# Kernel optimization log

Hardware: AMD Instinct MI355X
Metric: run time of the kernel (lower is better)

The kernel has to match this reference:

```python
import jax, jax.numpy as jnp
import numpy as np
import math

B, S, U, H = 2, 2048, 1024, 16
DK = U // H  # 64


def setup_inputs() -> dict:
    key = jax.random.key(0)
    ks = jax.random.split(key, 12)
    scale = 1.0 / math.sqrt(U)
    inp = {
        "query": jax.random.normal(ks[0], (B, S, U), dtype=jnp.float32),
        "key": jax.random.normal(ks[1], (B, S, U), dtype=jnp.float32),
        "value": jax.random.normal(ks[2], (B, S, U), dtype=jnp.float32),
        # causal mask, broadcast over batch: 1 = attend, 0 = masked
        "mask": jnp.broadcast_to(jnp.tril(jnp.ones((S, S), dtype=bool)), (B, S, S)),
        # nn.Linear params (torch convention: y = x @ W.T + b)
        "Wq": jax.random.uniform(ks[3], (U, U), jnp.float32, -scale, scale),
        "bq": jax.random.uniform(ks[4], (U,), jnp.float32, -scale, scale),
        "Wk": jax.random.uniform(ks[5], (U, U), jnp.float32, -scale, scale),
        "bk": jax.random.uniform(ks[6], (U,), jnp.float32, -scale, scale),
        "Wv": jax.random.uniform(ks[7], (U, U), jnp.float32, -scale, scale),
        "bv": jax.random.uniform(ks[8], (U,), jnp.float32, -scale, scale),
        "Wo": jax.random.uniform(ks[9], (U, U), jnp.float32, -scale, scale),
        "bo": jax.random.uniform(ks[10], (U,), jnp.float32, -scale, scale),
    }
    return inp


def reference(query, key, value, mask, Wq, bq, Wk, bk, Wv, bv, Wo, bo):
    b = query.shape[0]
    # QKV projections -> [b, H, S, DK]
    q = (query @ Wq.T + bq).reshape(b, -1, H, DK).transpose(0, 2, 1, 3)
    k = (key @ Wk.T + bk).reshape(b, -1, H, DK).transpose(0, 2, 1, 3)
    v = (value @ Wv.T + bv).reshape(b, -1, H, DK).transpose(0, 2, 1, 3)
    # scaled dot-product scores [b, H, Sq, Sk]
    scores = jnp.einsum("bhqd,bhkd->bhqk", q, k) / math.sqrt(DK)
    scores = jnp.where(mask[:, None, :, :], scores, jnp.float32(-1e9))
    A = jax.nn.softmax(scores, axis=-1)
    # dropout is eval/identity (p effectively inactive in reference)
    Hout = jnp.einsum("bhqk,bhkd->bhqd", A, v)
    H_concat = Hout.transpose(0, 2, 1, 3).reshape(b, -1, U)
    return H_concat @ Wo.T + bo
```

## Files before the change

kernel.cpp:

```cpp
#include <hip/hip_runtime.h>
#include <math.h>

#define B_NUM 2
#define S_LEN 2048
#define U_DIM 1024
#define H_NUM 16
#define DK 64
#define M_TOT (B_NUM * S_LEN)

typedef __attribute__((ext_vector_type(8))) short bf8;
typedef __attribute__((ext_vector_type(4))) float f4;

__device__ __forceinline__ unsigned short f2bf(float f) {
    union { float f; unsigned int u; } x; x.f = f;
    unsigned int r = x.u + 0x7fffu + ((x.u >> 16) & 1u);
    return (unsigned short)(r >> 16);
}

__device__ __forceinline__ void gl2lds16(const void* g, void* l) {
    __builtin_amdgcn_global_load_lds(
        (const __attribute__((address_space(1))) unsigned int*)g,
        (__attribute__((address_space(3))) unsigned int*)l, 16, 0, 0);
}

struct CvtArgs {
    const float* src[7];
    unsigned short* dst[7];
    int n[7];
};

__global__ __launch_bounds__(256) void convert_bf16(CvtArgs a)
{
    const int seg = blockIdx.y;
    const int i = (blockIdx.x * 256 + threadIdx.x) * 8;
    if (i >= a.n[seg]) return;
    const float* s = a.src[seg] + i;
    float4 v0 = *(const float4*)s;
    float4 v1 = *(const float4*)(s + 4);
    unsigned int p0 = (unsigned)f2bf(v0.x) | ((unsigned)f2bf(v0.y) << 16);
    unsigned int p1 = (unsigned)f2bf(v0.z) | ((unsigned)f2bf(v0.w) << 16);
    unsigned int p2 = (unsigned)f2bf(v1.x) | ((unsigned)f2bf(v1.y) << 16);
    unsigned int p3 = (unsigned)f2bf(v1.z) | ((unsigned)f2bf(v1.w) << 16);
    uint4 o = {p0, p1, p2, p3};
    *(uint4*)(a.dst[seg] + i) = o;
}

struct GemmLds {
    unsigned short As[2][128][32];
    unsigned short Bs[2][128][32];
};

template <int OMODE>
__device__ __forceinline__ void gemm_core(
    GemmLds& S,
    const unsigned short* __restrict__ A, const unsigned short* __restrict__ W,
    const float* __restrict__ bias, void* __restrict__ Cv, float scale,
    int bx, int by)
{
    const int tid = threadIdx.x;
    const int w = tid >> 6, lane = tid & 63;
    const int quad = lane >> 4, cid = lane & 15;
    const int wy = w >> 1, wx = w & 1;
    const int m0 = by * 128, n0 = bx * 128;

    const int row_s = tid >> 1;
    const int sp = tid & 1;
    const int rr = (row_s >> 2) & 3;
    const int p0 = (2 * sp + rr) & 3;
    const int p1 = (2 * sp + 1 + rr) & 3;

    const unsigned short* gA = A + (size_t)(m0 + row_s) * U_DIM + 16 * sp;
    const unsigned short* gB = W + (size_t)(n0 + row_s) * U_DIM + 16 * sp;

    uint4 a0, a1, b0, b1;
#define GPF(k0_) do {                                   \
        a0 = *(const uint4*)(gA + (k0_));               \
        a1 = *(const uint4*)(gA + (k0_) + 8);           \
        b0 = *(const uint4*)(gB + (k0_));               \
        b1 = *(const uint4*)(gB + (k0_) + 8);           \
    } while (0)

    f4 acc[4][4] = {};

    GPF(0);
    *(uint4*)&S.As[0][row_s][p0 * 8] = a0;
    *(uint4*)&S.As[0][row_s][p1 * 8] = a1;
    *(uint4*)&S.Bs[0][row_s][p0 * 8] = b0;
    *(uint4*)&S.Bs[0][row_s][p1 * 8] = b1;
    GPF(32);
    __syncthreads();

#pragma unroll 2
    for (int k0 = 0; k0 < U_DIM; k0 += 32) {
        const int cur = (k0 >> 5) & 1;
        if (k0 + 32 < U_DIM) {
            const int nxt = cur ^ 1;
            *(uint4*)&S.As[nxt][row_s][p0 * 8] = a0;
            *(uint4*)&S.As[nxt][row_s][p1 * 8] = a1;
            *(uint4*)&S.Bs[nxt][row_s][p0 * 8] = b0;
            *(uint4*)&S.Bs[nxt][row_s][p1 * 8] = b1;
            if (k0 + 64 < U_DIM) GPF(k0 + 64);
        }

        bf8 af[4], bfr[4];
#pragma unroll
        for (int mt = 0; mt < 4; ++mt) {
            int row = wy * 64 + mt * 16 + cid;
            int seg = (quad + (row >> 2)) & 3;
            af[mt] = *(const bf8*)&S.As[cur][row][seg * 8];
        }
#pragma unroll
        for (int nt = 0; nt < 4; ++nt) {
            int row = wx * 64 + nt * 16 + cid;
            int seg = (quad + (row >> 2)) & 3;
            bfr[nt] = *(const bf8*)&S.Bs[cur][row][seg * 8];
        }
#pragma unroll
        for (int mt = 0; mt < 4; ++mt)
#pragma unroll
            for (int nt = 0; nt < 4; ++nt)
                acc[mt][nt] = __builtin_amdgcn_mfma_f32_16x16x32_bf16(
                    af[mt], bfr[nt], acc[mt][nt], 0, 0, 0);
        __syncthreads();
    }
#undef GPF

#pragma unroll
    for (int nt = 0; nt < 4; ++nt) {
        int col = n0 + wx * 64 + nt * 16 + cid;
        float bv = bias[col];
#pragma unroll
        for (int mt = 0; mt < 4; ++mt) {
            int rowb = m0 + wy * 64 + mt * 16 + quad * 4;
#pragma unroll
            for (int i = 0; i < 4; ++i) {
                float v = (acc[mt][nt][i] + bv) * scale;
                if constexpr (OMODE == 0) {
                    ((unsigned short*)Cv)[(size_t)(rowb + i) * U_DIM + col] = f2bf(v);
                } else if constexpr (OMODE == 1) {
                    ((float*)Cv)[(size_t)(rowb + i) * U_DIM + col] = v;
                } else {
                    int bb = rowb >> 11;
                    int ss = (rowb & (S_LEN - 1)) + i;
                    size_t idx = ((size_t)(bb * H_NUM + (col >> 6)) * DK + (col & 63))
                                 * S_LEN + ss;
                    ((unsigned short*)Cv)[idx] = f2bf(v);
                }
            }
        }
    }
}

struct QkvArgs {
    const unsigned short* A[3];
    const unsigned short* W[3];
    const float* bias[3];
    unsigned short* C[3];
    float scale[3];
};

__global__ __launch_bounds__(256, 3) void gemm_qkv(QkvArgs a) {
    __shared__ GemmLds S;
    const int L = (int)blockIdx.x + 8 * ((int)blockIdx.y + 32 * (int)blockIdx.z);
    const int xcd = L & 7, j = L >> 3;
    const int z = j >> 5, r = j & 31;
    const int by = xcd * 4 + (r & 3);
    const int bx = r >> 2;
    if (z == 2)
        gemm_core<2>(S, a.A[2], a.W[2], a.bias[2], a.C[2], a.scale[2], bx, by);
    else
        gemm_core<0>(S, a.A[z], a.W[z], a.bias[z], a.C[z], a.scale[z], bx, by);
}

__global__ __launch_bounds__(256, 3) void gemm_obf(
    const unsigned short* __restrict__ A, const unsigned short* __restrict__ W,
    const float* __restrict__ bias, float* __restrict__ C) {
    __shared__ GemmLds S;
    const int L = (int)blockIdx.x + 8 * (int)blockIdx.y;
    const int xcd = L & 7, j = L >> 3;
    const int by = xcd * 4 + (j & 3);
    const int bx = j >> 2;
    gemm_core<1>(S, A, W, bias, C, 1.0f, bx, by);
}

__global__ __launch_bounds__(256, 3) void attn_mfma(
    const unsigned short* __restrict__ Q, const unsigned short* __restrict__ K,
    const unsigned short* __restrict__ VT, unsigned short* __restrict__ O)
{
    __shared__ __align__(16) unsigned short Ks[128][64];
    __shared__ __align__(16) unsigned short Vs[64][128];
    __shared__ __align__(16) unsigned short Ps[4][16][72];

    const int L = (int)blockIdx.x + 32 * ((int)blockIdx.y + 16 * (int)blockIdx.z);
    const int xcd = L & 7;
    const int j   = L >> 3;
    const int gl  = j & 3;
    const int i   = j >> 2;
    const int hb  = (xcd << 2) | gl;
    const int h = hb & 15, b = hb >> 4;
    const int qt = 31 - i;

    const int q0 = qt * 64;
    const int tid = threadIdx.x, w = tid >> 6, lane = tid & 63;
    const int quad = lane >> 4, cid = lane & 15;

#define KFRAG(r, s) (*(const bf8*)&Ks[r][(((s) ^ ((r) & 7)) * 8)])
#define VFRAG(r, s) (*(const bf8*)&Vs[r][(((((s) & 8) | (((s) ^ (r)) & 7))) * 8)])

    unsigned short (*QsA)[64] = (unsigned short (*)[64])&Ps[0][0][0];
    const int srow8 = lane >> 3;
    const int sw = ((lane & 7) ^ srow8) * 8;
    {
        const unsigned short* qg =
            Q + ((size_t)b * S_LEN + q0 + w * 16 + srow8) * U_DIM + h * DK + sw;
        gl2lds16(qg, &QsA[w * 16][0]);
        gl2lds16(qg + 8 * U_DIM, &QsA[w * 16 + 8][0]);
    }
    __syncthreads();
    const bf8 qfa = *(const bf8*)&QsA[w * 16 + cid][(((quad) ^ (cid & 7)) * 8)];
    const bf8 qfb = *(const bf8*)&QsA[w * 16 + cid][((((quad + 4)) ^ (cid & 7)) * 8)];

    const unsigned short* kgl =
        K + ((size_t)b * S_LEN + w * 32 + srow8) * U_DIM + h * DK + (lane & 7) * 8;
    const int vr0 = lane >> 4;
    const int s16 = lane & 15;
    const unsigned short* vgl =
        VT + ((size_t)(b * H_NUM + h) * DK + w * 16 + vr0) * S_LEN + s16 * 8;
    const int spE = (((s16 & 8) | ((s16 ^ vr0) & 7))) * 8;
    const int spO = (((s16 & 8) | ((s16 ^ (vr0 + 4)) & 7))) * 8;
    const int ksw = ((lane & 7) ^ srow8) * 8;

    uint4 kr0, kr1, kr2, kr3, vq0, vq1, vq2, vq3;
#define PREFETCH(kt_) do {                                                    \
        const unsigned short* kp_ = kgl + (size_t)(kt_) * 128 * U_DIM;        \
        kr0 = *(const uint4*)(kp_);                                           \
        kr1 = *(const uint4*)(kp_ + (size_t)8 * U_DIM);                       \
        kr2 = *(const uint4*)(kp_ + (size_t)16 * U_DIM);                      \
        kr3 = *(const uint4*)(kp_ + (size_t)24 * U_DIM);                      \
        const unsigned short* vp_ = vgl + (kt_) * 128;                        \
        vq0 = *(const uint4*)(vp_);                                           \
        vq1 = *(const uint4*)(vp_ + (size_t)4 * S_LEN);                       \
        vq2 = *(const uint4*)(vp_ + (size_t)8 * S_LEN);                       \
        vq3 = *(const uint4*)(vp_ + (size_t)12 * S_LEN);                      \
    } while (0)

    f4 o[4] = {};
    float l_i[4] = {0.0f, 0.0f, 0.0f, 0.0f};

    const int nkt = (qt >> 1) + 1;
    PREFETCH(0);

    for (int kt = 0; kt < nkt; ++kt) {
        __syncthreads();
        *(uint4*)&Ks[w * 32 + 0  + srow8][ksw] = kr0;
        *(uint4*)&Ks[w * 32 + 8  + srow8][ksw] = kr1;
        *(uint4*)&Ks[w * 32 + 16 + srow8][ksw] = kr2;
        *(uint4*)&Ks[w * 32 + 24 + srow8][ksw] = kr3;
        *(uint4*)&Vs[w * 16 + 0  + vr0][spE] = vq0;
        *(uint4*)&Vs[w * 16 + 4  + vr0][spO] = vq1;
        *(uint4*)&Vs[w * 16 + 8  + vr0][spE] = vq2;
        *(uint4*)&Vs[w * 16 + 12 + vr0][spO] = vq3;
        __syncthreads();
        if (kt + 1 < nkt) PREFETCH(kt + 1);

        f4 sc[8];
#pragma unroll
        for (int t = 0; t < 8; ++t) {
            int r = t * 16 + cid;
            f4 a = {};
            a = __builtin_amdgcn_mfma_f32_16x16x32_bf16(qfa, KFRAG(r, quad), a, 0, 0, 0);
            a = __builtin_amdgcn_mfma_f32_16x16x32_bf16(qfb, KFRAG(r, quad + 4), a, 0, 0, 0);
            sc[t] = a;
        }

        if (kt == nkt - 1) {
#pragma unroll
            for (int t = 0; t < 8; ++t) {
                int col = kt * 128 + t * 16 + cid;
#pragma unroll
                for (int i2 = 0; i2 < 4; ++i2) {
                    int row = q0 + w * 16 + quad * 4 + i2;
                    if (col > row) sc[t][i2] = -1e30f;
                }
            }
        }

#pragma unroll
        for (int i2 = 0; i2 < 4; ++i2) {
#pragma unroll
            for (int t = 0; t < 8; ++t) {
                float p = exp2f(sc[t][i2]);
                sc[t][i2] = p;
                l_i[i2] += p;
            }
        }

#pragma unroll
        for (int t = 0; t < 4; ++t)
#pragma unroll
            for (int i2 = 0; i2 < 4; ++i2)
                Ps[w][quad * 4 + i2][t * 16 + cid] = f2bf(sc[t][i2]);
        {
            bf8 pA0 = *(const bf8*)&Ps[w][cid][quad * 8];
            bf8 pA1 = *(const bf8*)&Ps[w][cid][32 + quad * 8];
#pragma unroll
            for (int t = 0; t < 4; ++t) {
                int r = t * 16 + cid;
                o[t] = __builtin_amdgcn_mfma_f32_16x16x32_bf16(pA0, VFRAG(r, quad), o[t], 0, 0, 0);
                o[t] = __builtin_amdgcn_mfma_f32_16x16x32_bf16(pA1, VFRAG(r, 4 + quad), o[t], 0, 0, 0);
            }
        }
#pragma unroll
        for (int t = 0; t < 4; ++t)
#pragma unroll
            for (int i2 = 0; i2 < 4; ++i2)
                Ps[w][quad * 4 + i2][t * 16 + cid] = f2bf(sc[4 + t][i2]);
        {
            bf8 pB0 = *(const bf8*)&Ps[w][cid][quad * 8];
            bf8 pB1 = *(const bf8*)&Ps[w][cid][32 + quad * 8];
#pragma unroll
            for (int t = 0; t < 4; ++t) {
                int r = t * 16 + cid;
                o[t] = __builtin_amdgcn_mfma_f32_16x16x32_bf16(pB0, VFRAG(r, 8 + quad), o[t], 0, 0, 0);
                o[t] = __builtin_amdgcn_mfma_f32_16x16x32_bf16(pB1, VFRAG(r, 12 + quad), o[t], 0, 0, 0);
            }
        }
    }
#undef PREFETCH
#undef KFRAG
#undef VFRAG

#pragma unroll
    for (int i2 = 0; i2 < 4; ++i2) {
        float l = l_i[i2];
        l += __shfl_xor(l, 1);
        l += __shfl_xor(l, 2);
        l += __shfl_xor(l, 4);
        l += __shfl_xor(l, 8);
        float inv = 1.0f / l;
        int rowg = q0 + w * 16 + quad * 4 + i2;
        size_t rbase = ((size_t)b * S_LEN + rowg) * U_DIM + h * DK;
#pragma unroll
        for (int t = 0; t < 4; ++t)
            O[rbase + t * 16 + cid] = f2bf(o[t][i2] * inv);
    }
}

extern "C" void kernel_launch(void* const* d_in, const int* in_sizes, int n_in,
                              void* d_out, int out_size, void* d_ws, size_t ws_size,
                              hipStream_t stream)
{
    const float* query = (const float*)d_in[0];
    const float* key   = (const float*)d_in[1];
    const float* value = (const float*)d_in[2];
    const float* Wq = (const float*)d_in[4];
    const float* bq = (const float*)d_in[5];
    const float* Wk = (const float*)d_in[6];
    const float* bk = (const float*)d_in[7];
    const float* Wv = (const float*)d_in[8];
    const float* bv = (const float*)d_in[9];
    const float* Wo = (const float*)d_in[10];
    const float* bo = (const float*)d_in[11];
    float* out = (float*)d_out;

    const size_t ACT = (size_t)M_TOT * U_DIM;
    const size_t WT  = (size_t)U_DIM * U_DIM;

    unsigned short* xq  = (unsigned short*)d_ws;
    unsigned short* xk  = xq + ACT;
    unsigned short* xv  = xk + ACT;
    unsigned short* wqb = xv + ACT;
    unsigned short* wkb = wqb + WT;
    unsigned short* wvb = wkb + WT;
    unsigned short* wob = wvb + WT;
    unsigned short* qg  = wob + WT;
    unsigned short* kg  = qg + ACT;
    unsigned short* vg  = kg + ACT;
    unsigned short* vt  = vg + ACT;
    unsigned short* ao  = vt + ACT;

    CvtArgs ca;
    ca.src[0] = query; ca.dst[0] = xq;  ca.n[0] = (int)ACT;
    ca.src[1] = key;   ca.dst[1] = xk;  ca.n[1] = (int)ACT;
    ca.src[2] = value; ca.dst[2] = xv;  ca.n[2] = (int)ACT;
    ca.src[3] = Wq;    ca.dst[3] = wqb; ca.n[3] = (int)WT;
    ca.src[4] = Wk;    ca.dst[4] = wkb; ca.n[4] = (int)WT;
    ca.src[5] = Wv;    ca.dst[5] = wvb; ca.n[5] = (int)WT;
    ca.src[6] = Wo;    ca.dst[6] = wob; ca.n[6] = (int)WT;
    convert_bf16<<<dim3(ACT / (256 * 8), 7), 256, 0, stream>>>(ca);

    QkvArgs ga;
    ga.A[0] = xq; ga.W[0] = wqb; ga.bias[0] = bq; ga.C[0] = qg;
    ga.scale[0] = 0.125f * 1.44269504088896340736f;
    ga.A[1] = xk; ga.W[1] = wkb; ga.bias[1] = bk; ga.C[1] = kg; ga.scale[1] = 1.0f;
    ga.A[2] = xv; ga.W[2] = wvb; ga.bias[2] = bv; ga.C[2] = vt; ga.scale[2] = 1.0f;
    gemm_qkv<<<dim3(U_DIM / 128, M_TOT / 128, 3), 256, 0, stream>>>(ga);

    attn_mfma<<<dim3(S_LEN / 64, H_NUM, B_NUM), 256, 0, stream>>>(qg, kg, vt, ao);

    gemm_obf<<<dim3(U_DIM / 128, M_TOT / 128), 256, 0, stream>>>(ao, wob, bo, out);
}
```

Before: 235.6 us.

## Compute transposed scores and shuffle P in registers instead of through LDS

The QK^T MFMA operands are swapped so each lane holds scores for one query row across keys. The probabilities are then packed to bf16 with v_cvt_pk_bf16_f32 and rearranged into MFMA A-operand layout with permlane32_swap and ds_swizzle, which removes the Ps LDS round-trip and its LDS traffic. Q staging now reuses the Ks buffer and launch bounds rise to 4 blocks per SU for more occupancy. The q-tile ordering is also changed to interleave long and short causal tiles for load balance. The risk is extra register pressure under the tighter launch bound and correctness of the hand-written permutation.

```diff
diff --git a/kernel.cpp b/kernel.cpp
--- a/kernel.cpp
+++ b/kernel.cpp
@@ -183,13 +183,12 @@
     gemm_core<1>(S, A, W, bias, C, 1.0f, bx, by);
 }
 
-__global__ __launch_bounds__(256, 3) void attn_mfma(
+__global__ __launch_bounds__(256, 4) void attn_mfma(
     const unsigned short* __restrict__ Q, const unsigned short* __restrict__ K,
     const unsigned short* __restrict__ VT, unsigned short* __restrict__ O)
 {
     __shared__ __align__(16) unsigned short Ks[128][64];
     __shared__ __align__(16) unsigned short Vs[64][128];
-    __shared__ __align__(16) unsigned short Ps[4][16][72];
 
     const int L = (int)blockIdx.x + 32 * ((int)blockIdx.y + 16 * (int)blockIdx.z);
     const int xcd = L & 7;
@@ -198,7 +197,9 @@
     const int i   = j >> 2;
     const int hb  = (xcd << 2) | gl;
     const int h = hb & 15, b = hb >> 4;
-    const int qt = 31 - i;
+    const int px = i & 7, pk = i >> 3;
+    const int qt = (pk == 0) ? 31 - px : (pk == 1) ? 16 + px
+                 : (pk == 2) ? 15 - px : px;
 
     const int q0 = qt * 64;
     const int tid = threadIdx.x, w = tid >> 6, lane = tid & 63;
@@ -207,7 +208,7 @@
 #define KFRAG(r, s) (*(const bf8*)&Ks[r][(((s) ^ ((r) & 7)) * 8)])
 #define VFRAG(r, s) (*(const bf8*)&Vs[r][(((((s) & 8) | (((s) ^ (r)) & 7))) * 8)])
 
-    unsigned short (*QsA)[64] = (unsigned short (*)[64])&Ps[0][0][0];
+    unsigned short (*QsA)[64] = (unsigned short (*)[64])&Ks[0][0];
     const int srow8 = lane >> 3;
     const int sw = ((lane & 7) ^ srow8) * 8;
     {
@@ -245,7 +246,8 @@
     } while (0)
 
     f4 o[4] = {};
-    float l_i[4] = {0.0f, 0.0f, 0.0f, 0.0f};
+    float l_p = 0.0f;
+    const int qrow = q0 + w * 16 + cid;
 
     const int nkt = (qt >> 1) + 1;
     PREFETCH(0);
@@ -268,61 +270,63 @@
         for (int t = 0; t < 8; ++t) {
             int r = t * 16 + cid;
             f4 a = {};
-            a = __builtin_amdgcn_mfma_f32_16x16x32_bf16(qfa, KFRAG(r, quad), a, 0, 0, 0);
-            a = __builtin_amdgcn_mfma_f32_16x16x32_bf16(qfb, KFRAG(r, quad + 4), a, 0, 0, 0);
+            a = __builtin_amdgcn_mfma_f32_16x16x32_bf16(KFRAG(r, quad), qfa, a, 0, 0, 0);
+            a = __builtin_amdgcn_mfma_f32_16x16x32_bf16(KFRAG(r, quad + 4), qfb, a, 0, 0, 0);
             sc[t] = a;
         }
 
         if (kt == nkt - 1) {
 #pragma unroll
             for (int t = 0; t < 8; ++t) {
-                int col = kt * 128 + t * 16 + cid;
 #pragma unroll
                 for (int i2 = 0; i2 < 4; ++i2) {
-                    int row = q0 + w * 16 + quad * 4 + i2;
-                    if (col > row) sc[t][i2] = -1e30f;
+                    int key = kt * 128 + t * 16 + quad * 4 + i2;
+                    if (key > qrow) sc[t][i2] = -1e30f;
                 }
             }
         }
 
 #pragma unroll
-        for (int i2 = 0; i2 < 4; ++i2) {
-#pragma unroll
-            for (int t = 0; t < 8; ++t) {
+        for (int t = 0; t < 8; ++t) {
+#pragma unroll
+            for (int i2 = 0; i2 < 4; ++i2) {
                 float p = exp2f(sc[t][i2]);
                 sc[t][i2] = p;
-                l_i[i2] += p;
+                l_p += p;
             }
         }
 
-#pragma unroll
-        for (int t = 0; t < 4; ++t)
-#pragma unroll
-            for (int i2 = 0; i2 < 4; ++i2)
-                Ps[w][quad * 4 + i2][t * 16 + cid] = f2bf(sc[t][i2]);
-        {
-            bf8 pA0 = *(const bf8*)&Ps[w][cid][quad * 8];
-            bf8 pA1 = *(const bf8*)&Ps[w][cid][32 + quad * 8];
+        unsigned int r_[8], r2_[8];
+#pragma unroll
+        for (int t = 0; t < 8; ++t) {
+            asm("v_cvt_pk_bf16_f32 %0, %1, %2"
+                : "=v"(r_[t]) : "v"(sc[t][0]), "v"(sc[t][1]));
+            asm("v_cvt_pk_bf16_f32 %0, %1, %2"
+                : "=v"(r2_[t]) : "v"(sc[t][2]), "v"(sc[t][3]));
+        }
+
+        const bool qodd = (quad & 1) != 0;
+#pragma unroll
+        for (int f = 0; f < 4; ++f) {
+            unsigned int xa = r_[2 * f], ya = r_[2 * f + 1];
+            asm("v_permlane32_swap_b32 %0, %1" : "+v"(xa), "+v"(ya));
+            unsigned int xas = __builtin_amdgcn_ds_swizzle((int)xa, 0x401f);
+            unsigned int yas = __builtin_amdgcn_ds_swizzle((int)ya, 0x401f);
+            unsigned int xb = r2_[2 * f], yb = r2_[2 * f + 1];
+            asm("v_permlane32_swap_b32 %0, %1" : "+v"(xb), "+v"(yb));
+            unsigned int xbs = __builtin_amdgcn_ds_swizzle((int)xb, 0x401f);
+            unsigned int ybs = __builtin_amdgcn_ds_swizzle((int)yb, 0x401f);
+            unsigned int u0 = qodd ? yas : xa;
+            unsigned int u1 = qodd ? ybs : xb;
+            unsigned int u2 = qodd ? ya : xas;
+            unsigned int u3 = qodd ? yb : xbs;
+            union { uint4 u; bf8 v; } pf;
+            pf.u = (uint4){u0, u1, u2, u3};
 #pragma unroll
             for (int t = 0; t < 4; ++t) {
                 int r = t * 16 + cid;
-                o[t] = __builtin_amdgcn_mfma_f32_16x16x32_bf16(pA0, VFRAG(r, quad), o[t], 0, 0, 0);
-                o[t] = __builtin_amdgcn_mfma_f32_16x16x32_bf16(pA1, VFRAG(r, 4 + quad), o[t], 0, 0, 0);
-            }
-        }
-#pragma unroll
-        for (int t = 0; t < 4; ++t)
-#pragma unroll
-            for (int i2 = 0; i2 < 4; ++i2)
-                Ps[w][quad * 4 + i2][t * 16 + cid] = f2bf(sc[4 + t][i2]);
-        {
-            bf8 pB0 = *(const bf8*)&Ps[w][cid][quad * 8];
-            bf8 pB1 = *(const bf8*)&Ps[w][cid][32 + quad * 8];
-#pragma unroll
-            for (int t = 0; t < 4; ++t) {
-                int r = t * 16 + cid;
-                o[t] = __builtin_amdgcn_mfma_f32_16x16x32_bf16(pB0, VFRAG(r, 8 + quad), o[t], 0, 0, 0);
-                o[t] = __builtin_amdgcn_mfma_f32_16x16x32_bf16(pB1, VFRAG(r, 12 + quad), o[t], 0, 0, 0);
+                o[t] = __builtin_amdgcn_mfma_f32_16x16x32_bf16(
+                    pf.v, VFRAG(r, 4 * f + quad), o[t], 0, 0, 0);
             }
         }
     }
@@ -330,19 +334,18 @@
 #undef KFRAG
 #undef VFRAG
 
+    float l = l_p;
+    l += __shfl_xor(l, 16);
+    l += __shfl_xor(l, 32);
+    const float inv = 1.0f / l;
 #pragma unroll
     for (int i2 = 0; i2 < 4; ++i2) {
-        float l = l_i[i2];
-        l += __shfl_xor(l, 1);
-        l += __shfl_xor(l, 2);
-        l += __shfl_xor(l, 4);
-        l += __shfl_xor(l, 8);
-        float inv = 1.0f / l;
+        float invi = __shfl(inv, (lane & 48) | (quad * 4 + i2));
         int rowg = q0 + w * 16 + quad * 4 + i2;
         size_t rbase = ((size_t)b * S_LEN + rowg) * U_DIM + h * DK;
 #pragma unroll
         for (int t = 0; t < 4; ++t)
-            O[rbase + t * 16 + cid] = f2bf(o[t][i2] * inv);
+            O[rbase + t * 16 + cid] = f2bf(o[t][i2] * invi);
     }
 }
 
```

Result: faster. 224.6 us (-4.7%).
